# Performance work log

Measured on AMD Instinct MI355X. Metric: run time of the kernel, lower is better.

Reference implementation:

```python
import jax, jax.numpy as jnp
import numpy as np

B, C, H, W = 8, 256, 160, 160

def setup_inputs() -> dict:
    key = jax.random.key(0)
    kx, kw, kh = jax.random.split(key, 3)
    x = jax.random.normal(kx, (B, C, H, W), dtype=jnp.float32)
    # kaiming_normal fan_in, relu -> std = sqrt(2/fan_in)
    fcw_w = jax.random.normal(kw, (1, W), dtype=jnp.float32) * np.float32(np.sqrt(2.0 / W))
    fch_w = jax.random.normal(kh, (1, H), dtype=jnp.float32) * np.float32(np.sqrt(2.0 / H))
    fcw_b = jnp.zeros((1,), dtype=jnp.float32)
    fch_b = jnp.zeros((1,), dtype=jnp.float32)
    return {"x": x, "fcw_w": fcw_w, "fcw_b": fcw_b, "fch_w": fch_w, "fch_b": fch_b}

def reference(x, fcw_w, fcw_b, fch_w, fch_b):
    b, c, h, w = x.shape
    xr = x.reshape(b * c, h, w)                                   # (n,h,w)
    # fc_w: Linear(w,1) then softmax over h (dim=1 of (n,h,1))
    alpha = jax.nn.softmax(jnp.einsum('nhw,w->nh', xr, fcw_w[0]) + fcw_b[0], axis=1)  # (n,h)
    # repeat+bmm == broadcasting a softmax-weighted row-sum to every row:
    # x_c[n,i,:] = sum_h alpha[n,h] * x[n,h,:]  (same for all i)
    row = jnp.einsum('nh,nhw->nw', alpha, xr)                      # (n,w)
    # fc_h on x_c^T (n,w,h): each h-column of x_c^T equals row, so the
    # Linear(h,1) reduces to row * sum(fch_w) + bias (identical math)
    beta = jax.nn.softmax(row * jnp.sum(fch_w[0]) + fch_b[0], axis=1)  # (n,w)
    # second repeat+bmm collapses to a scalar per (b,c): sum_w beta*row
    s = jnp.einsum('nw,nw->n', beta, row)                          # (n,)
    out = jnp.broadcast_to(s[:, None, None], (b * c, h, w)).reshape(b, c, h, w)
    return out
```

## Files before the change

kernel.cpp:

```cpp
#include <hip/hip_runtime.h>


#define HH 160
#define WW 160
#define NPLANE (HH * WW)
#define BLOCK 320
#define QN 40
#define PSTR 41

#define HALF 80
#define RPTH 10
#define WSSTR 164

typedef float f32x4 __attribute__((ext_vector_type(4)));

__global__ void __launch_bounds__(BLOCK, 7) sa1_part(
    const float* __restrict__ x,
    const float* __restrict__ fcw_w,
    float* __restrict__ ws)
{
    const int bid = blockIdx.x;
    const int n = bid >> 1;
    const int g = bid & 1;
    const int t = threadIdx.x;
    const int q = t % QN;
    const int v = t / QN;

    __shared__ float pbuf[HALF * PSTR];
    __shared__ float larr[HALF];
    __shared__ float sc[2];

    const float* xp = x + (size_t)n * NPLANE + (size_t)g * HALF * WW;

    const float4 ww = *(const float4*)(fcw_w + 4 * q);

    f32x4 xr[RPTH];
#pragma unroll
    for (int r = 0; r < RPTH; ++r)
        xr[r] = __builtin_nontemporal_load(
            (const f32x4*)(xp + (size_t)(v * RPTH + r) * WW + 4 * q));
#pragma unroll
    for (int r = 0; r < RPTH; ++r) {
        float p = xr[r].x * ww.x + xr[r].y * ww.y + xr[r].z * ww.z + xr[r].w * ww.w;
        pbuf[(v * RPTH + r) * PSTR + q] = p;
    }
    __syncthreads();

    {
        const int row = t >> 2;
        const int seg = t & 3;
        const float* pr = pbuf + row * PSTR + seg * 10;
        float s0 = 0.f, s1 = 0.f;
#pragma unroll
        for (int i = 0; i < 10; i += 2) { s0 += pr[i]; s1 += pr[i + 1]; }
        float hs = s0 + s1;
        hs += __shfl_xor(hs, 1, 64);
        hs += __shfl_xor(hs, 2, 64);
        if (seg == 0) larr[row] = hs;
    }
    __syncthreads();

    if (t < 32) {
        const float l0 = larr[t];
        const float l1 = larr[t + 32];
        const float l2 = (t < 16) ? larr[t + 64] : -3.0e38f;
        float m = fmaxf(l0, fmaxf(l1, l2));
#pragma unroll
        for (int off = 16; off >= 1; off >>= 1)
            m = fmaxf(m, __shfl_down(m, off, 32));
        m = __shfl(m, 0, 32);
        float z = __expf(l0 - m) + __expf(l1 - m) + __expf(l2 - m);
#pragma unroll
        for (int off = 16; off >= 1; off >>= 1)
            z += __shfl_down(z, off, 32);
        if (t == 0) { sc[0] = m; sc[1] = z; }
    }
    __syncthreads();

    const float m = sc[0];
    float4 rp = make_float4(0.f, 0.f, 0.f, 0.f);
#pragma unroll
    for (int r = 0; r < RPTH; ++r) {
        const float a = __expf(larr[v * RPTH + r] - m);
        rp.x += a * xr[r].x; rp.y += a * xr[r].y;
        rp.z += a * xr[r].z; rp.w += a * xr[r].w;
    }
    *(float4*)(pbuf + v * WW + 4 * q) = rp;
    __syncthreads();

    float* wsr = ws + (size_t)bid * WSSTR;
    if (t < WW) {
        float rs = 0.f;
#pragma unroll
        for (int vv = 0; vv < 8; ++vv) rs += pbuf[vv * WW + t];
        wsr[t] = rs;
    }
    if (t == 0) { wsr[160] = sc[0]; wsr[161] = sc[1]; }
}

#define BBLK 256
#define BIT (NPLANE / 4 / BBLK)

__global__ void __launch_bounds__(BBLK) sa1_bcast_merge(
    const float* __restrict__ ws,
    const float* __restrict__ fch_w,
    float* __restrict__ out)
{
    const int n = blockIdx.x;
    const int t = threadIdx.x;
    __shared__ float sc[2];

    float rv[5];
    if (t < 32) {
        const float* r0 = ws + (size_t)(2 * n) * WSSTR;
        const float* r1 = ws + (size_t)(2 * n + 1) * WSSTR;
        const float m0 = r0[160], z0 = r0[161];
        const float m1 = r1[160], z1 = r1[161];
        const float mm = fmaxf(m0, m1);
        const float f0 = __expf(m0 - mm);
        const float f1 = __expf(m1 - mm);
        const float rcpZ = 1.0f / (f0 * z0 + f1 * z1);
#pragma unroll
        for (int j = 0; j < 5; ++j) {
            const int w = t + 32 * j;
            rv[j] = (f0 * r0[w] + f1 * r1[w]) * rcpZ;
        }
    } else if (t >= 64 && t < 96) {
        const int u = t - 64;
        float s = 0.f;
#pragma unroll
        for (int j = 0; j < 5; ++j) s += fch_w[u + 32 * j];
#pragma unroll
        for (int off = 16; off >= 1; off >>= 1)
            s += __shfl_down(s, off, 32);
        if (u == 0) sc[0] = s;
    }
    __syncthreads();

    if (t < 32) {
        const float S = sc[0];
        float bl[5];
#pragma unroll
        for (int j = 0; j < 5; ++j) bl[j] = rv[j] * S;
        float mb = bl[0];
#pragma unroll
        for (int j = 1; j < 5; ++j) mb = fmaxf(mb, bl[j]);
#pragma unroll
        for (int off = 16; off >= 1; off >>= 1)
            mb = fmaxf(mb, __shfl_down(mb, off, 32));
        mb = __shfl(mb, 0, 32);
        float zb = 0.f, sd = 0.f;
#pragma unroll
        for (int j = 0; j < 5; ++j) {
            float e = __expf(bl[j] - mb);
            zb += e; sd += e * rv[j];
        }
#pragma unroll
        for (int off = 16; off >= 1; off >>= 1) {
            zb += __shfl_down(zb, off, 32);
            sd += __shfl_down(sd, off, 32);
        }
        if (t == 0) sc[1] = sd / zb;
    }
    __syncthreads();

    const float sv = sc[1];
    const f32x4 o = { sv, sv, sv, sv };
    float* op = out + (size_t)n * NPLANE;
#pragma unroll
    for (int i = 0; i < BIT; ++i)
        __builtin_nontemporal_store(
            o, (f32x4*)(op + 4 * (size_t)(i * BBLK + threadIdx.x)));
}

#define RPT 20

__global__ void __launch_bounds__(BLOCK, 4) sa1_reduce(
    const float* __restrict__ x,
    const float* __restrict__ fcw_w,
    const float* __restrict__ fch_w,
    float* __restrict__ s_out)
{
    const int n = blockIdx.x;
    const int t = threadIdx.x;
    const int q = t % QN;
    const int v = t / QN;

    __shared__ float pbuf[HH * PSTR];
    __shared__ float larrA[HH];
    __shared__ float larrB[HH];
    __shared__ float sc[4];

    const float* xp = x + (size_t)n * NPLANE;
    const float4 ww = *(const float4*)(fcw_w + 4 * q);

    f32x4 xr[RPT];
#pragma unroll
    for (int r = 0; r < RPT; ++r)
        xr[r] = __builtin_nontemporal_load(
            (const f32x4*)(xp + (size_t)(v * RPT + r) * WW + 4 * q));
#pragma unroll
    for (int r = 0; r < RPT; ++r) {
        float p = xr[r].x * ww.x + xr[r].y * ww.y + xr[r].z * ww.z + xr[r].w * ww.w;
        pbuf[(v * RPT + r) * PSTR + q] = p;
    }
    __syncthreads();

    {
        const int h = (t < HH) ? t : (t - HH);
        const int qb = (t < HH) ? 0 : (QN / 2);
        const float* pr = pbuf + h * PSTR + qb;
        float s0 = 0.f, s1 = 0.f, s2 = 0.f, s3 = 0.f;
#pragma unroll
        for (int qq = 0; qq < QN / 2; qq += 4) {
            s0 += pr[qq]; s1 += pr[qq + 1]; s2 += pr[qq + 2]; s3 += pr[qq + 3];
        }
        float hs = (s0 + s1) + (s2 + s3);
        if (t < HH) larrA[h] = hs; else larrB[h] = hs;
    }
    __syncthreads();

    if (t < 32) {
        float lv[5];
#pragma unroll
        for (int j = 0; j < 5; ++j) lv[j] = larrA[t + 32 * j] + larrB[t + 32 * j];
        float m = lv[0];
#pragma unroll
        for (int j = 1; j < 5; ++j) m = fmaxf(m, lv[j]);
#pragma unroll
        for (int off = 16; off >= 1; off >>= 1)
            m = fmaxf(m, __shfl_down(m, off, 32));
        m = __shfl(m, 0, 32);
        float z = 0.f;
#pragma unroll
        for (int j = 0; j < 5; ++j) z += __expf(lv[j] - m);
#pragma unroll
        for (int off = 16; off >= 1; off >>= 1)
            z += __shfl_down(z, off, 32);
        if (t == 0) { sc[0] = m; sc[1] = z; }
    } else if (t >= 64 && t < 96) {
        const int u = t - 64;
        float s = 0.f;
#pragma unroll
        for (int j = 0; j < 5; ++j) s += fch_w[u + 32 * j];
#pragma unroll
        for (int off = 16; off >= 1; off >>= 1)
            s += __shfl_down(s, off, 32);
        if (u == 0) sc[2] = s;
    }
    __syncthreads();

    const float m = sc[0];
    float4 rp = make_float4(0.f, 0.f, 0.f, 0.f);
#pragma unroll
    for (int r = 0; r < RPT; ++r) {
        const int h = v * RPT + r;
        const float a = __expf((larrA[h] + larrB[h]) - m);
        rp.x += a * xr[r].x; rp.y += a * xr[r].y;
        rp.z += a * xr[r].z; rp.w += a * xr[r].w;
    }
    *(float4*)(pbuf + v * WW + 4 * q) = rp;
    __syncthreads();

    if (t < 32) {
        const float S = sc[2];
        const float rcpZ = 1.0f / sc[1];
        float rv[5], bl[5];
#pragma unroll
        for (int j = 0; j < 5; ++j) {
            const int w = t + 32 * j;
            float rs = 0.f;
#pragma unroll
            for (int vv = 0; vv < 8; ++vv) rs += pbuf[vv * WW + w];
            rv[j] = rs * rcpZ;
            bl[j] = rv[j] * S;
        }
        float mb = bl[0];
#pragma unroll
        for (int j = 1; j < 5; ++j) mb = fmaxf(mb, bl[j]);
#pragma unroll
        for (int off = 16; off >= 1; off >>= 1)
            mb = fmaxf(mb, __shfl_down(mb, off, 32));
        mb = __shfl(mb, 0, 32);
        float zb = 0.f, sd = 0.f;
#pragma unroll
        for (int j = 0; j < 5; ++j) {
            float e = __expf(bl[j] - mb);
            zb += e; sd += e * rv[j];
        }
#pragma unroll
        for (int off = 16; off >= 1; off >>= 1) {
            zb += __shfl_down(zb, off, 32);
            sd += __shfl_down(sd, off, 32);
        }
        if (t == 0) s_out[n] = sd / zb;
    }
}

__global__ void __launch_bounds__(BBLK) sa1_bcast(
    const float* __restrict__ s, float* __restrict__ out)
{
    const int n = blockIdx.x;
    const float sv = s[n];
    const f32x4 o = { sv, sv, sv, sv };
    float* op = out + (size_t)n * NPLANE;
#pragma unroll
    for (int i = 0; i < BIT; ++i)
        __builtin_nontemporal_store(
            o, (f32x4*)(op + 4 * (size_t)(i * BBLK + threadIdx.x)));
}

extern "C" void kernel_launch(void* const* d_in, const int* in_sizes, int n_in,
                              void* d_out, int out_size, void* d_ws, size_t ws_size,
                              hipStream_t stream) {
    const float* x     = (const float*)d_in[0];
    const float* fcw_w = (const float*)d_in[1];
    const float* fch_w = (const float*)d_in[3];
    float* out = (float*)d_out;

    const int nplanes = 8 * 256;
    const size_t need = (size_t)(2 * nplanes) * WSSTR * sizeof(float);

    if (ws_size >= need) {
        float* wsp = (float*)d_ws;
        sa1_part<<<2 * nplanes, BLOCK, 0, stream>>>(x, fcw_w, wsp);
        sa1_bcast_merge<<<nplanes, BBLK, 0, stream>>>(wsp, fch_w, out);
    } else {
        float* svec = (float*)d_ws;
        sa1_reduce<<<nplanes, BLOCK, 0, stream>>>(x, fcw_w, fch_w, svec);
        sa1_bcast<<<nplanes, BBLK, 0, stream>>>(svec, out);
    }
}
```

Measured before the change: 341.5 us.

## Fuse partial reduction and broadcast merge via last-block atomic counter

Merges the two-kernel path (half-plane partial softmax reduction, then merge and broadcast) into one kernel. Each plane's second-finishing block, detected through an agent-scope atomic counter, merges the two partials, computes the scalar and writes the broadcast output. This removes a kernel launch and the gap between the two passes, so output stores can overlap with other blocks' reads. In exchange it adds a hipMemsetAsync to zero the counters, a threadfence plus atomic per block, and concentrates the output writes in half of the blocks.

```diff
diff --git a/kernel.cpp b/kernel.cpp
--- a/kernel.cpp
+++ b/kernel.cpp
@@ -11,13 +11,17 @@
 #define HALF 80
 #define RPTH 10
 #define WSSTR 164
+#define NPL 2048
 
 typedef float f32x4 __attribute__((ext_vector_type(4)));
 
-__global__ void __launch_bounds__(BLOCK, 7) sa1_part(
+__global__ void __launch_bounds__(BLOCK, 7) sa1_fused(
     const float* __restrict__ x,
     const float* __restrict__ fcw_w,
-    float* __restrict__ ws)
+    const float* __restrict__ fch_w,
+    unsigned int* __restrict__ cnt,
+    float* __restrict__ ws,
+    float* __restrict__ out)
 {
     const int bid = blockIdx.x;
     const int n = bid >> 1;
@@ -28,7 +32,8 @@
 
     __shared__ float pbuf[HALF * PSTR];
     __shared__ float larr[HALF];
-    __shared__ float sc[2];
+    __shared__ float sc[4];
+    __shared__ int lastf;
 
     const float* xp = x + (size_t)n * NPLANE + (size_t)g * HALF * WW;
 
@@ -74,6 +79,15 @@
         for (int off = 16; off >= 1; off >>= 1)
             z += __shfl_down(z, off, 32);
         if (t == 0) { sc[0] = m; sc[1] = z; }
+    } else if (t >= 64 && t < 96) {
+        const int u = t - 64;
+        float s = 0.f;
+#pragma unroll
+        for (int j = 0; j < 5; ++j) s += fch_w[u + 32 * j];
+#pragma unroll
+        for (int off = 16; off >= 1; off >>= 1)
+            s += __shfl_down(s, off, 32);
+        if (u == 0) sc[2] = s;
     }
     __syncthreads();
 
@@ -96,52 +110,34 @@
         wsr[t] = rs;
     }
     if (t == 0) { wsr[160] = sc[0]; wsr[161] = sc[1]; }
-}
-
-#define BBLK 256
-#define BIT (NPLANE / 4 / BBLK)
-
-__global__ void __launch_bounds__(BBLK) sa1_bcast_merge(
-    const float* __restrict__ ws,
-    const float* __restrict__ fch_w,
-    float* __restrict__ out)
-{
-    const int n = blockIdx.x;
-    const int t = threadIdx.x;
-    __shared__ float sc[2];
-
-    float rv[5];
+    __syncthreads();
+
+    if (t == 0) {
+        __threadfence();
+        unsigned int old = __hip_atomic_fetch_add(
+            &cnt[n], 1u, __ATOMIC_ACQ_REL, __HIP_MEMORY_SCOPE_AGENT);
+        lastf = (old == 1);
+    }
+    __syncthreads();
+    if (!lastf) return;
+
+    const float* r0 = ws + (size_t)(2 * n) * WSSTR;
+    const float* r1 = r0 + WSSTR;
     if (t < 32) {
-        const float* r0 = ws + (size_t)(2 * n) * WSSTR;
-        const float* r1 = ws + (size_t)(2 * n + 1) * WSSTR;
         const float m0 = r0[160], z0 = r0[161];
         const float m1 = r1[160], z1 = r1[161];
         const float mm = fmaxf(m0, m1);
         const float f0 = __expf(m0 - mm);
         const float f1 = __expf(m1 - mm);
         const float rcpZ = 1.0f / (f0 * z0 + f1 * z1);
+        const float S = sc[2];
+        float rv[5], bl[5];
 #pragma unroll
         for (int j = 0; j < 5; ++j) {
             const int w = t + 32 * j;
             rv[j] = (f0 * r0[w] + f1 * r1[w]) * rcpZ;
-        }
-    } else if (t >= 64 && t < 96) {
-        const int u = t - 64;
-        float s = 0.f;
-#pragma unroll
-        for (int j = 0; j < 5; ++j) s += fch_w[u + 32 * j];
-#pragma unroll
-        for (int off = 16; off >= 1; off >>= 1)
-            s += __shfl_down(s, off, 32);
-        if (u == 0) sc[0] = s;
-    }
-    __syncthreads();
-
-    if (t < 32) {
-        const float S = sc[0];
-        float bl[5];
-#pragma unroll
-        for (int j = 0; j < 5; ++j) bl[j] = rv[j] * S;
+            bl[j] = rv[j] * S;
+        }
         float mb = bl[0];
 #pragma unroll
         for (int j = 1; j < 5; ++j) mb = fmaxf(mb, bl[j]);
@@ -160,20 +156,22 @@
             zb += __shfl_down(zb, off, 32);
             sd += __shfl_down(sd, off, 32);
         }
-        if (t == 0) sc[1] = sd / zb;
-    }
-    __syncthreads();
-
-    const float sv = sc[1];
+        if (t == 0) sc[3] = sd / zb;
+    }
+    __syncthreads();
+
+    const float sv = sc[3];
     const f32x4 o = { sv, sv, sv, sv };
     float* op = out + (size_t)n * NPLANE;
 #pragma unroll
-    for (int i = 0; i < BIT; ++i)
+    for (int i = 0; i < 20; ++i)
         __builtin_nontemporal_store(
-            o, (f32x4*)(op + 4 * (size_t)(i * BBLK + threadIdx.x)));
+            o, (f32x4*)(op + 4 * (size_t)(i * BLOCK + t)));
 }
 
 #define RPT 20
+#define BBLK 256
+#define BIT (NPLANE / 4 / BBLK)
 
 __global__ void __launch_bounds__(BLOCK, 4) sa1_reduce(
     const float* __restrict__ x,
@@ -318,16 +316,17 @@
     const float* fch_w = (const float*)d_in[3];
     float* out = (float*)d_out;
 
-    const int nplanes = 8 * 256;
-    const size_t need = (size_t)(2 * nplanes) * WSSTR * sizeof(float);
+    const size_t cntBytes = (size_t)NPL * sizeof(unsigned int);
+    const size_t need = cntBytes + (size_t)(2 * NPL) * WSSTR * sizeof(float);
 
     if (ws_size >= need) {
-        float* wsp = (float*)d_ws;
-        sa1_part<<<2 * nplanes, BLOCK, 0, stream>>>(x, fcw_w, wsp);
-        sa1_bcast_merge<<<nplanes, BBLK, 0, stream>>>(wsp, fch_w, out);
+        unsigned int* cnt = (unsigned int*)d_ws;
+        float* wsp = (float*)((char*)d_ws + cntBytes);
+        hipMemsetAsync(d_ws, 0, cntBytes, stream);
+        sa1_fused<<<2 * NPL, BLOCK, 0, stream>>>(x, fcw_w, fch_w, cnt, wsp, out);
     } else {
         float* svec = (float*)d_ws;
-        sa1_reduce<<<nplanes, BLOCK, 0, stream>>>(x, fcw_w, fch_w, svec);
-        sa1_bcast<<<nplanes, BBLK, 0, stream>>>(svec, out);
+        sa1_reduce<<<NPL, BLOCK, 0, stream>>>(x, fcw_w, fch_w, svec);
+        sa1_bcast<<<NPL, BBLK, 0, stream>>>(svec, out);
     }
 }
```

New measurement: 729.2 us. 2.14x slower.
